# Optimization experiments

Hardware: AMD Instinct MI355X
Metric: run time of the kernel (lower is better)

Reference implementation:

```python
import jax, jax.numpy as jnp
import numpy as np

NUM_HEADS = 16


def setup_inputs() -> dict:
    key = jax.random.key(0)
    ks = jax.random.split(key, 10)
    B, S, D = 2, 2048, 1024
    x = jax.random.normal(ks[0], (B, S, D), dtype=jnp.float32)
    mask = jax.random.randint(ks[1], (B, 1, 1, S), 0, 2, dtype=jnp.int32)
    scale = 1.0 / np.sqrt(D)
    wq = jax.random.normal(ks[2], (D, D), dtype=jnp.float32) * scale
    bq = jnp.zeros((D,), dtype=jnp.float32)
    wk = jax.random.normal(ks[3], (D, D), dtype=jnp.float32) * scale
    bk = jnp.zeros((D,), dtype=jnp.float32)
    wv = jax.random.normal(ks[4], (D, D), dtype=jnp.float32) * scale
    bv = jnp.zeros((D,), dtype=jnp.float32)
    wo = jax.random.normal(ks[5], (D, D), dtype=jnp.float32) * scale
    bo = jnp.zeros((D,), dtype=jnp.float32)
    return {"x": x, "mask": mask, "wq": wq, "bq": bq, "wk": wk, "bk": bk,
            "wv": wv, "bv": bv, "wo": wo, "bo": bo}


def reference(x, mask, wq, bq, wk, bk, wv, bv, wo, bo):
    B, S, D = x.shape
    H = NUM_HEADS
    dk = D // H

    def split_heads(t):
        # (B, S, D) -> (B, H, S, dk)
        return t.reshape(B, S, H, dk).transpose(0, 2, 1, 3)

    # PyTorch nn.Linear: y = x @ W^T + b
    q = split_heads(x @ wq.T + bq)
    k = split_heads(x @ wk.T + bk)
    v = split_heads(x @ wv.T + bv)

    # scaled dot-product attention with explicit score matrix (as original)
    logits = jnp.einsum('bhqd,bhkd->bhqk', q, k) / jnp.sqrt(jnp.float32(dk))
    logits = jnp.where(mask == 0, jnp.float32(-1e9), logits)
    attn_weights = jax.nn.softmax(logits, axis=-1)
    # dropout(p=0.1) is identity in eval mode (deterministic reference)
    attn = jnp.einsum('bhqk,bhkd->bhqd', attn_weights, v)

    attn = attn.transpose(0, 2, 1, 3).reshape(B, S, D)
    out = attn @ wo.T + bo
    return out, attn_weights
```

## Files before the change

### kernel.cpp

```cpp
#include <hip/hip_runtime.h>
#include <hip/hip_bf16.h>

#define DEV __device__ __forceinline__

typedef __attribute__((ext_vector_type(8))) __bf16 bf16x8;
typedef __attribute__((ext_vector_type(8))) short s16x8;
typedef __attribute__((ext_vector_type(4))) float f32x4;
typedef __attribute__((ext_vector_type(2))) unsigned long long u64x2;

DEV f32x4 mfma16(s16x8 a, s16x8 b, f32x4 c){
  return __builtin_amdgcn_mfma_f32_16x16x32_bf16(
      __builtin_bit_cast(bf16x8, a), __builtin_bit_cast(bf16x8, b), c, 0, 0, 0);
}

DEV unsigned int cvtpk(float a, float b){
  float2 t; t.x = a; t.y = b;
  __hip_bfloat162 h = __float22bfloat162_rn(t);
  unsigned int r;
  __builtin_memcpy(&r, &h, 4);
  return r;
}

DEV unsigned short f2bf(float f){
  __hip_bfloat16 h = __float2bfloat16(f);
  unsigned short r;
  __builtin_memcpy(&r, &h, 2);
  return r;
}

DEV float bf2f(unsigned short u){
  return __builtin_bit_cast(float, ((unsigned int)u) << 16);
}

DEV unsigned long long pack4(float4 v){
  return (unsigned long long)cvtpk(v.x, v.y) | ((unsigned long long)cvtpk(v.z, v.w) << 32);
}

DEV unsigned long long pack4f(float a, float b, float c, float d){
  return (unsigned long long)cvtpk(a, b) | ((unsigned long long)cvtpk(c, d) << 32);
}

DEV void async16(const void* g, void* l){
  __builtin_amdgcn_global_load_lds(
      (const __attribute__((address_space(1))) unsigned int*)g,
      (__attribute__((address_space(3))) unsigned int*)l, 16, 0, 0);
}

__global__ __launch_bounds__(256) void cvt_kernel(
    const float* __restrict__ x, const float* __restrict__ wq, const float* __restrict__ wk,
    const float* __restrict__ wv, const float* __restrict__ wo,
    const float* __restrict__ bq, const float* __restrict__ bk, const float* __restrict__ bv,
    unsigned long long* __restrict__ xb, unsigned long long* __restrict__ wqkvb,
    unsigned long long* __restrict__ wob, float4* __restrict__ bqkv)
{
  const int i = blockIdx.x * 256 + threadIdx.x;
  const int X4 = 1048576, W4 = 262144;
  if (i < X4){
    xb[i] = pack4(((const float4*)x)[i]);
  } else if (i < X4 + 3*W4){
    int j = i - X4;
    const float* src = (j < W4) ? wq : (j < 2*W4) ? wk : wv;
    int jj = (j < W4) ? j : (j < 2*W4) ? (j - W4) : (j - 2*W4);
    wqkvb[j] = pack4(((const float4*)src)[jj]);
  } else if (i < X4 + 4*W4){
    int j = i - X4 - 3*W4;
    wob[j] = pack4(((const float4*)wo)[j]);
  } else if (i < X4 + 4*W4 + 768){
    int j = i - X4 - 4*W4;
    const float* src = (j < 256) ? bq : (j < 512) ? bk : bv;
    int jj = (j < 256) ? j : (j < 512) ? (j - 256) : (j - 512);
    bqkv[j] = ((const float4*)src)[jj];
  }
}

__global__ __launch_bounds__(256) void gemm_qkv(
    const unsigned short* __restrict__ A,
    const unsigned short* __restrict__ B,
    const float* __restrict__ bias,
    unsigned short* __restrict__ oq,
    unsigned short* __restrict__ okk,
    unsigned short* __restrict__ ovt)
{
  __shared__ __align__(16) char smem[32768];
  char* As = smem;
  char* Bs = smem + 16384;
  const int tid = threadIdx.x;
  const int l = tid & 63, w = tid >> 6, g = l >> 4;

  const int orig = blockIdx.x;
  const int lin = (orig & 7) * 96 + (orig >> 3);
  const int m0 = (lin / 24) * 128, n0 = (lin % 24) * 128;
  const int rowbytes = 2048;

  f32x4 acc[4][4] = {};
  const int wr = w >> 1, wc = w & 1;
  const int wm = wr * 64, wn = wc * 64;

  const int srow = w * 32 + (l >> 3);
  const int scol = (((l & 7) ^ (l >> 3)) << 4);
  const char* Abp = (const char*)A + (size_t)(m0 + srow) * rowbytes + scol;
  const char* Bbp = (const char*)B + (size_t)(n0 + srow) * rowbytes + scol;
  char* Asw = As + w * 4096;
  char* Bsw = Bs + w * 4096;

  int aoff[4][2], boff[4][2];
  for (int mf = 0; mf < 4; ++mf)
    for (int ks = 0; ks < 2; ++ks){
      int ra = wm + mf * 16 + (l & 15);
      aoff[mf][ks] = ra * 128 + ((ks * 64 + g * 16) ^ ((l & 7) << 4));
      int rb = wn + mf * 16 + (l & 15);
      boff[mf][ks] = rb * 128 + ((ks * 64 + g * 16) ^ ((l & 7) << 4));
    }

  for (int kt = 0; kt < 16; ++kt){
    const char* ab = Abp + kt * 128;
    const char* bb = Bbp + kt * 128;
    for (int i = 0; i < 4; ++i){
      async16(ab + (size_t)i * 8 * rowbytes, Asw + i * 1024);
      async16(bb + (size_t)i * 8 * rowbytes, Bsw + i * 1024);
    }
    __syncthreads();
    for (int ks = 0; ks < 2; ++ks){
      s16x8 af[4], bf[4];
      for (int mf = 0; mf < 4; ++mf) af[mf] = *(const s16x8*)(As + aoff[mf][ks]);
      for (int nf = 0; nf < 4; ++nf) bf[nf] = *(const s16x8*)(Bs + boff[nf][ks]);
      for (int mf = 0; mf < 4; ++mf)
        for (int nf = 0; nf < 4; ++nf)
          acc[mf][nf] = mfma16(af[mf], bf[nf], acc[mf][nf]);
    }
    __syncthreads();
  }

  if (n0 >= 2048){
    for (int nf = 0; nf < 4; ++nf){
      int nloc = wn + nf * 16 + (l & 15);
      float bs = bias[n0 + nloc];
      for (int mf = 0; mf < 4; ++mf){
        int mby = (wm + mf * 16 + g * 4) * 2;
        unsigned long long pk = pack4f(acc[mf][nf][0] + bs, acc[mf][nf][1] + bs,
                                       acc[mf][nf][2] + bs, acc[mf][nf][3] + bs);
        *(unsigned long long*)(smem + nloc * 256 + (mby ^ ((nloc & 15) << 4))) = pk;
      }
    }
    __syncthreads();
    int b2 = m0 >> 11, s0 = m0 & 2047;
    for (int i = 0; i < 8; ++i){
      int idx = i * 256 + tid;
      int row = idx >> 4, c8 = (idx & 15) * 8;
      s16x8 vv = *(const s16x8*)(smem + row * 256 + ((c8 * 2) ^ ((row & 15) << 4)));
      *(s16x8*)(ovt + (size_t)(b2 * 1024 + (n0 - 2048) + row) * 2048 + s0 + c8) = vv;
    }
    return;
  }

  for (int mf = 0; mf < 4; ++mf)
    for (int nf = 0; nf < 4; ++nf)
      for (int r = 0; r < 4; ++r){
        int grow = m0 + wm + mf * 16 + g * 4 + r;
        int n = n0 + wn + nf * 16 + (l & 15);
        float v = acc[mf][nf][r] + bias[n];
        if (n < 1024) oq [(size_t)grow * 1024 + n]          = f2bf(v);
        else          okk[(size_t)grow * 1024 + (n - 1024)] = f2bf(v);
      }
}

__global__ __launch_bounds__(256) void gemm_out(
    const unsigned short* __restrict__ A,
    const unsigned short* __restrict__ B,
    const float* __restrict__ bias,
    float* __restrict__ of)
{
  __shared__ __align__(16) char smem[32768];
  char* As = smem;
  char* Bs = smem + 16384;
  const int tid = threadIdx.x, l = tid & 63, w = tid >> 6, g = l >> 4;
  const int orig = blockIdx.x;
  const int lin = (orig & 7) * 64 + (orig >> 3);
  const int m0 = (lin >> 4) * 128, n0 = (lin & 15) * 64;
  const int rowbytes = 2048;

  f32x4 acc[2][4] = {};
  const int wm = w * 32;

  const int scol = (((l & 7) ^ (l >> 3)) << 4);
  const char* Abp = (const char*)A + (size_t)(m0 + w * 32 + (l >> 3)) * rowbytes + scol;
  const char* Bbp = (const char*)B + (size_t)(n0 + w * 16 + (l >> 3)) * rowbytes + scol;
  char* Asw = As + w * 4096;
  char* Bsw = Bs + w * 2048;

  int aoff[2][2], boff[4][2];
  for (int ks = 0; ks < 2; ++ks){
    for (int mf = 0; mf < 2; ++mf){
      int ra = wm + mf * 16 + (l & 15);
      aoff[mf][ks] = ra * 128 + ((ks * 64 + g * 16) ^ ((l & 7) << 4));
    }
    for (int nf = 0; nf < 4; ++nf){
      int rb = nf * 16 + (l & 15);
      boff[nf][ks] = rb * 128 + ((ks * 64 + g * 16) ^ ((l & 7) << 4));
    }
  }

  for (int kt = 0; kt < 16; ++kt){
    for (int i = 0; i < 4; ++i)
      async16(Abp + kt * 128 + (size_t)i * 8 * rowbytes, Asw + i * 1024);
    for (int i = 0; i < 2; ++i)
      async16(Bbp + kt * 128 + (size_t)i * 8 * rowbytes, Bsw + i * 1024);
    __syncthreads();
    for (int ks = 0; ks < 2; ++ks){
      s16x8 af[2], bf[4];
      for (int mf = 0; mf < 2; ++mf) af[mf] = *(const s16x8*)(As + aoff[mf][ks]);
      for (int nf = 0; nf < 4; ++nf) bf[nf] = *(const s16x8*)(Bs + boff[nf][ks]);
      for (int mf = 0; mf < 2; ++mf)
        for (int nf = 0; nf < 4; ++nf)
          acc[mf][nf] = mfma16(af[mf], bf[nf], acc[mf][nf]);
    }
    __syncthreads();
  }

  __syncthreads();
  char* stg = smem + w * 8192;
  float bv4[4];
  for (int nf = 0; nf < 4; ++nf) bv4[nf] = bias[n0 + nf * 16 + (l & 15)];
  for (int mf = 0; mf < 2; ++mf)
    for (int nf = 0; nf < 4; ++nf)
      for (int r = 0; r < 4; ++r){
        int row = mf * 16 + g * 4 + r;
        int colb = (nf * 16 + (l & 15)) * 4;
        *(float*)(stg + row * 256 + (colb ^ ((row & 7) << 4))) = acc[mf][nf][r] + bv4[nf];
      }
  __syncthreads();
  for (int t = 0; t < 8; ++t){
    int row = t * 4 + (l >> 4);
    int colb = ((l & 15) * 16) ^ ((row & 7) << 4);
    f32x4 v = *(const f32x4*)(stg + row * 256 + colb);
    __builtin_nontemporal_store(v, (f32x4*)&of[(size_t)(m0 + wm + row) * 1024 + n0 + (l & 15) * 4]);
  }
}

__global__ __launch_bounds__(512) void attn_kernel(
    const unsigned short* __restrict__ qb,
    const unsigned short* __restrict__ kb,
    const unsigned short* __restrict__ vtb,
    const int* __restrict__ mask,
    float* __restrict__ Pout,
    unsigned short* __restrict__ attnb)
{
  const int flat = blockIdx.x;
  const int sw = (flat & 7) * 256 + (flat >> 3);
  const int qt = sw & 63, h = (sw >> 6) & 15, b = sw >> 10;
  const int tid = threadIdx.x, l = tid & 63, w = tid >> 6, g = l >> 4;
  const int q0 = qt * 32;

  __shared__ __align__(16) unsigned long long estu[16384];
  __shared__ float maskadd[2048];
  __shared__ float zpart[8][32];
  __shared__ float zfullinv[32];

  char* Ebase = (char*)estu;

  for (int i = tid; i < 2048; i += 512)
    maskadd[i] = mask[b * 2048 + i] ? 0.0f : -1e30f;

  s16x8 qf[2][2];
  for (int mf = 0; mf < 2; ++mf)
    for (int ks = 0; ks < 2; ++ks)
      qf[mf][ks] = *(const s16x8*)(qb + (size_t)(b*2048 + q0 + mf*16 + (l&15)) * 1024
                                   + h*64 + ks*32 + g*8);

  const unsigned short* Kb = kb + (size_t)b * 2048 * 1024 + h * 64;
  const unsigned short* Vb = vtb + ((size_t)b * 1024 + h * 64) * 2048;

  __syncthreads();

  float zacc[2] = {0.0f, 0.0f};
  for (int jj = 0; jj < 4; ++jj){
    const int kk0 = w * 256 + jj * 64;
    const int cb = kk0 * 2;
    f32x4 c[2][4] = {};
    for (int nh = 0; nh < 2; ++nh){
      s16x8 kf[2][2];
      for (int n2 = 0; n2 < 2; ++n2)
        for (int ks = 0; ks < 2; ++ks)
          kf[n2][ks] = *(const s16x8*)(Kb + (size_t)(kk0 + (nh*2+n2)*16 + (l&15)) * 1024 + ks*32 + g*8);
      __builtin_amdgcn_s_setprio(1);
      for (int ks = 0; ks < 2; ++ks)
        for (int mf = 0; mf < 2; ++mf)
          for (int n2 = 0; n2 < 2; ++n2)
            c[mf][nh*2+n2] = mfma16(kf[n2][ks], qf[mf][ks], c[mf][nh*2+n2]);
      __builtin_amdgcn_s_setprio(0);
    }
    for (int mf = 0; mf < 2; ++mf){
      int q = mf*16 + (l & 15);
      for (int nf = 0; nf < 4; ++nf){
        f32x4 ma = *(const f32x4*)&maskadd[kk0 + nf*16 + g*4];
        f32x4 e;
        for (int r = 0; r < 4; ++r){
          e[r] = __expf(fmaf(c[mf][nf][r], 0.125f, ma[r]));
          zacc[mf] += e[r];
        }
        *(unsigned long long*)(Ebase + q*4096 + cb + ((nf*32 + g*8) ^ ((q & 7) << 4))) =
            pack4f(e[0], e[1], e[2], e[3]);
      }
    }
  }
  for (int mf = 0; mf < 2; ++mf){
    float z = zacc[mf];
    z += __shfl_xor(z, 16, 64);
    z += __shfl_xor(z, 32, 64);
    zacc[mf] = z;
  }
  if (g == 0){
    zpart[w][l & 15]        = zacc[0];
    zpart[w][16 + (l & 15)] = zacc[1];
  }
  __syncthreads();
  if (tid < 32){
    float s = 0.0f;
    for (int ww = 0; ww < 8; ++ww) s += zpart[ww][tid];
    zfullinv[tid] = 1.0f / s;
  }
  __syncthreads();

  float* Pb = Pout + ((size_t)(b*16 + h) * 2048 + q0) * 2048;
  f32x4 pv[2][4] = {};
  for (int jj = 0; jj < 4; ++jj){
    const int kk0 = w * 256 + jj * 64;
    const int cb = kk0 * 2;
    s16x8 pa[2][2];
    for (int mf = 0; mf < 2; ++mf)
      for (int ks = 0; ks < 2; ++ks){
        int q = mf*16 + (l & 15);
        const unsigned long long* pp =
            (const unsigned long long*)(Ebase + q*4096 + cb + ((ks*64 + g*16) ^ ((q & 7) << 4)));
        u64x2 t; t[0] = pp[0]; t[1] = pp[1];
        pa[mf][ks] = __builtin_bit_cast(s16x8, t);
      }
    for (int dh = 0; dh < 2; ++dh){
      s16x8 vf[2][2];
      for (int d2 = 0; d2 < 2; ++d2)
        for (int ks = 0; ks < 2; ++ks)
          vf[d2][ks] = *(const s16x8*)(Vb + (size_t)((dh*2+d2)*16 + (l&15)) * 2048 + kk0 + ks*32 + g*8);
      __builtin_amdgcn_s_setprio(1);
      for (int ks = 0; ks < 2; ++ks)
        for (int mf = 0; mf < 2; ++mf)
          for (int d2 = 0; d2 < 2; ++d2)
            pv[mf][dh*2+d2] = mfma16(pa[mf][ks], vf[d2][ks], pv[mf][dh*2+d2]);
      __builtin_amdgcn_s_setprio(0);
    }
    for (int t = 0; t < 8; ++t){
      int row = t * 4 + (l >> 4);
      unsigned long long pk =
          *(const unsigned long long*)(Ebase + row*4096 + cb + (((l & 15) * 8) ^ ((row & 7) << 4)));
      float zr = zfullinv[row];
      f32x4 ps;
      ps[0] = bf2f((unsigned short)(pk      )) * zr;
      ps[1] = bf2f((unsigned short)(pk >> 16)) * zr;
      ps[2] = bf2f((unsigned short)(pk >> 32)) * zr;
      ps[3] = bf2f((unsigned short)(pk >> 48)) * zr;
      __builtin_nontemporal_store(ps, (f32x4*)&Pb[(size_t)row * 2048 + kk0 + (l & 15) * 4]);
    }
  }

  __syncthreads();
  char* bufw = Ebase + w * 8192;
  for (int mf = 0; mf < 2; ++mf)
    for (int dn = 0; dn < 4; ++dn)
      for (int r = 0; r < 4; ++r){
        int row = mf*16 + g*4 + r, col = dn*16 + (l & 15);
        *(float*)(bufw + row*256 + ((col*4) ^ (((row >> 2) & 3) << 6))) = pv[mf][dn][r];
      }
  __syncthreads();
  {
    int row = tid >> 4, c4 = (tid & 15) * 4;
    int off = row*256 + ((c4*4) ^ (((row >> 2) & 3) << 6));
    f32x4 s = {};
    for (int ww = 0; ww < 8; ++ww)
      s += *(const f32x4*)(Ebase + ww*8192 + off);
    float zr = zfullinv[row];
    unsigned long long ov = pack4f(s[0]*zr, s[1]*zr, s[2]*zr, s[3]*zr);
    *(unsigned long long*)&attnb[(size_t)(b*2048 + q0 + row) * 1024 + h*64 + c4] = ov;
  }
}

extern "C" void kernel_launch(void* const* d_in, const int* in_sizes, int n_in,
                              void* d_out, int out_size, void* d_ws, size_t ws_size,
                              hipStream_t stream)
{
  const float* x  = (const float*)d_in[0];
  const int* mask = (const int*)d_in[1];
  const float* wq = (const float*)d_in[2];
  const float* bq = (const float*)d_in[3];
  const float* wk = (const float*)d_in[4];
  const float* bk = (const float*)d_in[5];
  const float* wv = (const float*)d_in[6];
  const float* bv = (const float*)d_in[7];
  const float* wo = (const float*)d_in[8];
  const float* bo = (const float*)d_in[9];

  char* ws = (char*)d_ws;
  unsigned short* xb    = (unsigned short*)(ws);
  unsigned short* wqkvb = (unsigned short*)(ws + 8388608);
  unsigned short* wob   = (unsigned short*)(ws + 14680064);
  float*          bqkv  = (float*)(ws + 16777216);
  unsigned short* qb    = (unsigned short*)(ws + 16793600);
  unsigned short* kb    = (unsigned short*)(ws + 25182208);
  unsigned short* vtb   = (unsigned short*)(ws + 33570816);
  unsigned short* attnb = (unsigned short*)(ws + 41959424);

  float* fout = (float*)d_out;
  float* Pout = fout + 4194304;

  cvt_kernel<<<8195, 256, 0, stream>>>(x, wq, wk, wv, wo, bq, bk, bv,
                                       (unsigned long long*)xb, (unsigned long long*)wqkvb,
                                       (unsigned long long*)wob, (float4*)bqkv);
  gemm_qkv<<<768, 256, 0, stream>>>(xb, wqkvb, bqkv, qb, kb, vtb);
  attn_kernel<<<2048, 512, 0, stream>>>(qb, kb, vtb, mask, Pout, attnb);
  gemm_out<<<512, 256, 0, stream>>>(attnb, wob, bo, fout);
}
```

Measured before the change: 244.6 us.

## Split PV matmul by output tile across waves instead of key-split reduction

```diff
diff --git a/kernel.cpp b/kernel.cpp
--- a/kernel.cpp
+++ b/kernel.cpp
@@ -321,34 +321,37 @@
   }
   __syncthreads();
 
+  const int qi = w >> 2, di = w & 3;
+  const int ql = qi*16 + (l & 15);
+  const int qswz = ((ql & 7) << 4);
+  const unsigned short* Vrow = Vb + (size_t)(di*16 + (l&15)) * 2048;
+  f32x4 a4[4] = {};
+  for (int c4 = 0; c4 < 16; ++c4){
+#pragma unroll
+    for (int u = 0; u < 4; ++u){
+      const int c32 = c4*4 + u;
+      const unsigned long long* pp = (const unsigned long long*)
+          (Ebase + ql*4096 + (c32 >> 1)*128 + (((c32 & 1)*64 + g*16) ^ qswz));
+      u64x2 t2; t2[0] = pp[0]; t2[1] = pp[1];
+      s16x8 pa = __builtin_bit_cast(s16x8, t2);
+      s16x8 vf = *(const s16x8*)(Vrow + c32*32 + g*8);
+      a4[u] = mfma16(pa, vf, a4[u]);
+    }
+  }
+  f32x4 accf = a4[0] + a4[1] + a4[2] + a4[3];
+
+  for (int r = 0; r < 4; ++r){
+    int row = qi*16 + g*4 + r;
+    float zr = zfullinv[row];
+    attnb[(size_t)(b*2048 + q0 + row) * 1024 + h*64 + di*16 + (l & 15)] = f2bf(accf[r] * zr);
+  }
+
   float* Pb = Pout + ((size_t)(b*16 + h) * 2048 + q0) * 2048;
-  f32x4 pv[2][4] = {};
   for (int jj = 0; jj < 4; ++jj){
     const int kk0 = w * 256 + jj * 64;
     const int cb = kk0 * 2;
-    s16x8 pa[2][2];
-    for (int mf = 0; mf < 2; ++mf)
-      for (int ks = 0; ks < 2; ++ks){
-        int q = mf*16 + (l & 15);
-        const unsigned long long* pp =
-            (const unsigned long long*)(Ebase + q*4096 + cb + ((ks*64 + g*16) ^ ((q & 7) << 4)));
-        u64x2 t; t[0] = pp[0]; t[1] = pp[1];
-        pa[mf][ks] = __builtin_bit_cast(s16x8, t);
-      }
-    for (int dh = 0; dh < 2; ++dh){
-      s16x8 vf[2][2];
-      for (int d2 = 0; d2 < 2; ++d2)
-        for (int ks = 0; ks < 2; ++ks)
-          vf[d2][ks] = *(const s16x8*)(Vb + (size_t)((dh*2+d2)*16 + (l&15)) * 2048 + kk0 + ks*32 + g*8);
-      __builtin_amdgcn_s_setprio(1);
-      for (int ks = 0; ks < 2; ++ks)
-        for (int mf = 0; mf < 2; ++mf)
-          for (int d2 = 0; d2 < 2; ++d2)
-            pv[mf][dh*2+d2] = mfma16(pa[mf][ks], vf[d2][ks], pv[mf][dh*2+d2]);
-      __builtin_amdgcn_s_setprio(0);
-    }
     for (int t = 0; t < 8; ++t){
-      int row = t * 4 + (l >> 4);
+      int row = t * 4 + g;
       unsigned long long pk =
           *(const unsigned long long*)(Ebase + row*4096 + cb + (((l & 15) * 8) ^ ((row & 7) << 4)));
       float zr = zfullinv[row];
@@ -359,26 +362,6 @@
       ps[3] = bf2f((unsigned short)(pk >> 48)) * zr;
       __builtin_nontemporal_store(ps, (f32x4*)&Pb[(size_t)row * 2048 + kk0 + (l & 15) * 4]);
     }
-  }
-
-  __syncthreads();
-  char* bufw = Ebase + w * 8192;
-  for (int mf = 0; mf < 2; ++mf)
-    for (int dn = 0; dn < 4; ++dn)
-      for (int r = 0; r < 4; ++r){
-        int row = mf*16 + g*4 + r, col = dn*16 + (l & 15);
-        *(float*)(bufw + row*256 + ((col*4) ^ (((row >> 2) & 3) << 6))) = pv[mf][dn][r];
-      }
-  __syncthreads();
-  {
-    int row = tid >> 4, c4 = (tid & 15) * 4;
-    int off = row*256 + ((c4*4) ^ (((row >> 2) & 3) << 6));
-    f32x4 s = {};
-    for (int ww = 0; ww < 8; ++ww)
-      s += *(const f32x4*)(Ebase + ww*8192 + off);
-    float zr = zfullinv[row];
-    unsigned long long ov = pack4f(s[0]*zr, s[1]*zr, s[2]*zr, s[3]*zr);
-    *(unsigned long long*)&attnb[(size_t)(b*2048 + q0 + row) * 1024 + h*64 + c4] = ov;
   }
 }
 
```

Result: slower. 304.6 us (+24.5%).

## Enlarge QKV GEMM tile to 256x128 with 512-thread blocks

Applied to the files above, without the earlier changes.

```diff
diff --git a/kernel.cpp b/kernel.cpp
--- a/kernel.cpp
+++ b/kernel.cpp
@@ -73,7 +73,7 @@
   }
 }
 
-__global__ __launch_bounds__(256) void gemm_qkv(
+__global__ __launch_bounds__(512, 2) void gemm_qkv(
     const unsigned short* __restrict__ A,
     const unsigned short* __restrict__ B,
     const float* __restrict__ bias,
@@ -81,44 +81,42 @@
     unsigned short* __restrict__ okk,
     unsigned short* __restrict__ ovt)
 {
-  __shared__ __align__(16) char smem[32768];
+  __shared__ __align__(16) char smem[49152];
   char* As = smem;
-  char* Bs = smem + 16384;
+  char* Bs = smem + 32768;
   const int tid = threadIdx.x;
   const int l = tid & 63, w = tid >> 6, g = l >> 4;
 
   const int orig = blockIdx.x;
-  const int lin = (orig & 7) * 96 + (orig >> 3);
-  const int m0 = (lin / 24) * 128, n0 = (lin % 24) * 128;
+  const int lin = (orig & 7) * 48 + (orig >> 3);
+  const int m0 = (lin / 24) * 256, n0 = (lin % 24) * 128;
   const int rowbytes = 2048;
 
   f32x4 acc[4][4] = {};
   const int wr = w >> 1, wc = w & 1;
   const int wm = wr * 64, wn = wc * 64;
 
-  const int srow = w * 32 + (l >> 3);
+  const int srow = w * 8 + (l >> 3);
   const int scol = (((l & 7) ^ (l >> 3)) << 4);
   const char* Abp = (const char*)A + (size_t)(m0 + srow) * rowbytes + scol;
   const char* Bbp = (const char*)B + (size_t)(n0 + srow) * rowbytes + scol;
-  char* Asw = As + w * 4096;
-  char* Bsw = Bs + w * 4096;
 
   int aoff[4][2], boff[4][2];
-  for (int mf = 0; mf < 4; ++mf)
+  for (int f = 0; f < 4; ++f)
     for (int ks = 0; ks < 2; ++ks){
-      int ra = wm + mf * 16 + (l & 15);
-      aoff[mf][ks] = ra * 128 + ((ks * 64 + g * 16) ^ ((l & 7) << 4));
-      int rb = wn + mf * 16 + (l & 15);
-      boff[mf][ks] = rb * 128 + ((ks * 64 + g * 16) ^ ((l & 7) << 4));
+      int ra = wm + f * 16 + (l & 15);
+      aoff[f][ks] = ra * 128 + ((ks * 64 + g * 16) ^ ((l & 7) << 4));
+      int rb = wn + f * 16 + (l & 15);
+      boff[f][ks] = rb * 128 + ((ks * 64 + g * 16) ^ ((l & 7) << 4));
     }
 
   for (int kt = 0; kt < 16; ++kt){
     const char* ab = Abp + kt * 128;
     const char* bb = Bbp + kt * 128;
-    for (int i = 0; i < 4; ++i){
-      async16(ab + (size_t)i * 8 * rowbytes, Asw + i * 1024);
-      async16(bb + (size_t)i * 8 * rowbytes, Bsw + i * 1024);
-    }
+    for (int r = 0; r < 4; ++r)
+      async16(ab + (size_t)r * 64 * rowbytes, As + r * 8192 + w * 1024);
+    for (int r = 0; r < 2; ++r)
+      async16(bb + (size_t)r * 64 * rowbytes, Bs + r * 8192 + w * 1024);
     __syncthreads();
     for (int ks = 0; ks < 2; ++ks){
       s16x8 af[4], bf[4];
@@ -132,23 +130,28 @@
   }
 
   if (n0 >= 2048){
-    for (int nf = 0; nf < 4; ++nf){
-      int nloc = wn + nf * 16 + (l & 15);
-      float bs = bias[n0 + nloc];
-      for (int mf = 0; mf < 4; ++mf){
-        int mby = (wm + mf * 16 + g * 4) * 2;
-        unsigned long long pk = pack4f(acc[mf][nf][0] + bs, acc[mf][nf][1] + bs,
-                                       acc[mf][nf][2] + bs, acc[mf][nf][3] + bs);
-        *(unsigned long long*)(smem + nloc * 256 + (mby ^ ((nloc & 15) << 4))) = pk;
-      }
-    }
-    __syncthreads();
-    int b2 = m0 >> 11, s0 = m0 & 2047;
-    for (int i = 0; i < 8; ++i){
-      int idx = i * 256 + tid;
-      int row = idx >> 4, c8 = (idx & 15) * 8;
-      s16x8 vv = *(const s16x8*)(smem + row * 256 + ((c8 * 2) ^ ((row & 15) << 4)));
-      *(s16x8*)(ovt + (size_t)(b2 * 1024 + (n0 - 2048) + row) * 2048 + s0 + c8) = vv;
+    const int b2 = m0 >> 11, s0 = m0 & 2047;
+    for (int h2 = 0; h2 < 2; ++h2){
+      if (wr >> 1 == h2){
+        for (int nf = 0; nf < 4; ++nf){
+          int nloc = wn + nf * 16 + (l & 15);
+          float bs = bias[n0 + nloc];
+          for (int mf = 0; mf < 4; ++mf){
+            int mby = ((wr & 1) * 64 + mf * 16 + g * 4) * 2;
+            unsigned long long pk = pack4f(acc[mf][nf][0] + bs, acc[mf][nf][1] + bs,
+                                           acc[mf][nf][2] + bs, acc[mf][nf][3] + bs);
+            *(unsigned long long*)(As + nloc * 256 + (mby ^ ((nloc & 15) << 4))) = pk;
+          }
+        }
+      }
+      __syncthreads();
+      for (int it = 0; it < 4; ++it){
+        int idx = it * 512 + tid;
+        int drow = idx >> 4, c8 = (idx & 15) * 8;
+        s16x8 vv = *(const s16x8*)(As + drow * 256 + ((c8 * 2) ^ ((drow & 15) << 4)));
+        *(s16x8*)(ovt + (size_t)(b2 * 1024 + (n0 - 2048) + drow) * 2048 + s0 + h2 * 128 + c8) = vv;
+      }
+      __syncthreads();
     }
     return;
   }
@@ -413,7 +416,7 @@
   cvt_kernel<<<8195, 256, 0, stream>>>(x, wq, wk, wv, wo, bq, bk, bv,
                                        (unsigned long long*)xb, (unsigned long long*)wqkvb,
                                        (unsigned long long*)wob, (float4*)bqkv);
-  gemm_qkv<<<768, 256, 0, stream>>>(xb, wqkvb, bqkv, qb, kb, vtb);
+  gemm_qkv<<<384, 512, 0, stream>>>(xb, wqkvb, bqkv, qb, kb, vtb);
   attn_kernel<<<2048, 512, 0, stream>>>(qb, kb, vtb, mask, Pout, attnb);
   gemm_out<<<512, 256, 0, stream>>>(attnb, wob, bo, fout);
 }
```

Result: faster. 230.6 us, median of 2 (-5.7%).
